# Performance work log

Hardware: AMD Instinct MI355X
Metric: run time of the kernel (lower is better)

The kernel has to match this reference:

```python
import jax, jax.numpy as jnp
import numpy as np

EPS = 1e-5

def _bn(x, gamma, beta):
    # BatchNorm1d training-mode math: batch mean / biased variance over edge dim
    mean = jnp.mean(x, axis=0)
    var = jnp.mean(jnp.square(x - mean), axis=0)
    return (x - mean) * (gamma / jnp.sqrt(var + EPS)) + beta


def setup_inputs() -> dict:
    key = jax.random.key(0)
    ks = jax.random.split(key, 12)
    n, d, s, h, e = 50000, 256, 32, 128, 500000
    feat = 3 * d + s + 1  # 801
    sc = lambda fan_in: 1.0 / np.sqrt(fan_in)
    return {
        "node_embeddings": jax.random.normal(ks[0], (n, d), jnp.float32),
        "gradient_scores": jax.random.normal(ks[1], (e,), jnp.float32),
        "step_embedding": jax.random.normal(ks[2], (s,), jnp.float32),
        "W1": jax.random.normal(ks[3], (feat, h), jnp.float32) * sc(feat),
        "b1": jnp.zeros((h,), jnp.float32),
        "g1": jnp.ones((h,), jnp.float32),
        "be1": jnp.zeros((h,), jnp.float32),
        "W2": jax.random.normal(ks[4], (h, h // 2), jnp.float32) * sc(h),
        "b2": jnp.zeros((h // 2,), jnp.float32),
        "g2": jnp.ones((h // 2,), jnp.float32),
        "be2": jnp.zeros((h // 2,), jnp.float32),
        "W3": jax.random.normal(ks[5], (h // 2, 1), jnp.float32) * sc(h // 2),
        "b3": jnp.zeros((1,), jnp.float32),
        "edge_index": jax.random.randint(ks[6], (2, e), 0, n, jnp.int64),
    }


def reference(node_embeddings, gradient_scores, step_embedding,
              W1, b1, g1, be1, W2, b2, g2, be2, W3, b3, edge_index):
    src, dst = edge_index[0], edge_index[1]
    h_u = node_embeddings[src]              # [E, d]
    h_v = node_embeddings[dst]              # [E, d]
    edge_diff = jnp.abs(h_u - h_v)          # [E, d]
    E = edge_index.shape[1]
    step = jnp.broadcast_to(step_embedding[None, :], (E, step_embedding.shape[0]))
    feats = jnp.concatenate([h_u, h_v, edge_diff, step, gradient_scores[:, None]], axis=1)
    x = jnp.maximum(feats @ W1 + b1, 0.0)
    x = _bn(x, g1, be1)                     # dropout is identity in eval
    x = jnp.maximum(x @ W2 + b2, 0.0)
    x = _bn(x, g2, be2)
    out = jnp.tanh(x @ W3 + b3)[:, 0]       # [E]
    return out
```

## Files before the change

kernel.cpp:

```cpp
#include <hip/hip_runtime.h>

#define NE 500000
#define DIMK 256
#define H1 128
#define H2 64
#define EPSBN 1e-5f
#define GRID1 512
#define NT1 1954
#define NJOBS2 NT1

typedef _Float16 half8 __attribute__((ext_vector_type(8)));
typedef float f32x4 __attribute__((ext_vector_type(4)));
typedef unsigned short ushort8 __attribute__((ext_vector_type(8)));

static __device__ __forceinline__ half8 habs8(half8 x) {
  ushort8 u = __builtin_bit_cast(ushort8, x);
  u &= (unsigned short)0x7FFF;
  return __builtin_bit_cast(half8, u);
}
static __device__ __forceinline__ float h2f(unsigned int u) {
  return (float)__builtin_bit_cast(_Float16, (unsigned short)(u & 0xffff));
}

__global__ void k_prep(const float* __restrict__ W1, const float* __restrict__ b1,
                       const float* __restrict__ step, float* __restrict__ c0) {
  const int j = threadIdx.x;
  if (j < H1) {
    float a = b1[j];
#pragma unroll
    for (int tt = 0; tt < 32; ++tt) a += step[tt] * W1[(768 + tt) * H1 + j];
    c0[j] = a;
  }
}

__global__ void k_prep16(const float* __restrict__ emb, _Float16* __restrict__ embh) {
  const int i = (blockIdx.x * 256 + threadIdx.x) * 8;
  const float4 a = *(const float4*)(emb + i);
  const float4 b = *(const float4*)(emb + i + 4);
  half8 h;
  h[0] = (_Float16)a.x; h[1] = (_Float16)a.y; h[2] = (_Float16)a.z; h[3] = (_Float16)a.w;
  h[4] = (_Float16)b.x; h[5] = (_Float16)b.y; h[6] = (_Float16)b.z; h[7] = (_Float16)b.w;
  *(half8*)(embh + i) = h;
}

__global__ void k_prepB(const float* __restrict__ W1, _Float16* __restrict__ bfrag) {
  const int g = blockIdx.x * 256 + threadIdx.x;
  const int lane = g & 63, f = g >> 6;
  const int c = f & 7, kc = (f >> 3) & 7, s = f >> 6;
  const int row0 = s * 256 + kc * 32 + (lane >> 4) * 8;
  const int col = c * 16 + (lane & 15);
  half8 h;
#pragma unroll
  for (int j = 0; j < 8; ++j) h[j] = (_Float16)W1[(row0 + j) * H1 + col];
  *(half8*)(bfrag + (size_t)g * 8) = h;
}

__global__ __launch_bounds__(256, 2)
void k_layer1(const _Float16* __restrict__ embh, const void* __restrict__ eidx_raw,
              const float* __restrict__ grad, const float* __restrict__ W1,
              const float* __restrict__ c0, const _Float16* __restrict__ bfrag,
              _Float16* __restrict__ x1, float* __restrict__ p1) {
  __shared__ int s_src[256], s_dst[256];
  __shared__ float s_g[256];
  __shared__ float s_wg[128], s_c0[128], s_sum[128], s_sq[128];

  const int t = threadIdx.x, bid = blockIdx.x;
  const int w = t >> 6, lane = t & 63, quad = lane >> 4, m15 = lane & 15;

  if (t < 128) {
    s_wg[t] = W1[800 * H1 + t];
    s_c0[t] = c0[t];
    s_sum[t] = 0.f; s_sq[t] = 0.f;
  }

  const unsigned* ew = (const unsigned*)eidx_raw;
  const bool is64 = ((ew[1] | ew[3] | ew[5] | ew[7]) == 0u);
  const int* e32 = (const int*)eidx_raw;
  const long long* e64 = (const long long*)eidx_raw;

  float st_s[8] = {0, 0, 0, 0, 0, 0, 0, 0}, st_q[8] = {0, 0, 0, 0, 0, 0, 0, 0};
  const half8* bp = (const half8*)bfrag;

  for (int tile = bid; tile < NT1; tile += GRID1) {
    const int base = tile * 256;
    __syncthreads();
    {
      int e = base + t; if (e >= NE) e = NE - 1;
      if (is64) { s_src[t] = (int)e64[e]; s_dst[t] = (int)e64[NE + e]; }
      else      { s_src[t] = e32[e];      s_dst[t] = e32[NE + e]; }
      s_g[t] = grad[e];
    }
    __syncthreads();

    const int r0 = w * 64 + m15;
    const _Float16* pu[4];
    const _Float16* pv[4];
#pragma unroll
    for (int r = 0; r < 4; ++r) {
      pu[r] = embh + (size_t)s_src[r0 + r * 16] * DIMK + quad * 8;
      pv[r] = embh + (size_t)s_dst[r0 + r * 16] * DIMK + quad * 8;
    }
    f32x4 acc[4][8];
#pragma unroll
    for (int r = 0; r < 4; ++r)
#pragma unroll
      for (int c = 0; c < 8; ++c) acc[r][c] = (f32x4)0.f;

#pragma unroll 1
    for (int kc = 0; kc < 8; ++kc) {
      half8 u[4], v[4], d[4];
#pragma unroll
      for (int r = 0; r < 4; ++r) {
        u[r] = *(const half8*)(pu[r] + kc * 32);
        v[r] = *(const half8*)(pv[r] + kc * 32);
      }
#pragma unroll
      for (int r = 0; r < 4; ++r) d[r] = habs8(u[r] - v[r]);

      half8 bu = bp[(kc * 8 + 0) * 64 + lane];
      half8 bv = bp[(64 + kc * 8 + 0) * 64 + lane];
      half8 bd = bp[(128 + kc * 8 + 0) * 64 + lane];
#pragma unroll
      for (int c = 0; c < 8; ++c) {
        half8 nbu, nbv, nbd;
        if (c < 7) {
          nbu = bp[(kc * 8 + c + 1) * 64 + lane];
          nbv = bp[(64 + kc * 8 + c + 1) * 64 + lane];
          nbd = bp[(128 + kc * 8 + c + 1) * 64 + lane];
        }
#pragma unroll
        for (int r = 0; r < 4; ++r)
          acc[r][c] = __builtin_amdgcn_mfma_f32_16x16x32_f16(u[r], bu, acc[r][c], 0, 0, 0);
#pragma unroll
        for (int r = 0; r < 4; ++r)
          acc[r][c] = __builtin_amdgcn_mfma_f32_16x16x32_f16(v[r], bv, acc[r][c], 0, 0, 0);
#pragma unroll
        for (int r = 0; r < 4; ++r)
          acc[r][c] = __builtin_amdgcn_mfma_f32_16x16x32_f16(d[r], bd, acc[r][c], 0, 0, 0);
        if (c < 7) { bu = nbu; bv = nbv; bd = nbd; }
      }
    }
#pragma unroll
    for (int r = 0; r < 4; ++r) {
      const int erow = w * 64 + r * 16 + quad * 4;
#pragma unroll
      for (int c = 0; c < 8; ++c) {
        const int colL = c * 16 + m15;
        const float wgv = s_wg[colL], c0v = s_c0[colL];
#pragma unroll
        for (int reg = 0; reg < 4; ++reg) {
          const int e = base + erow + reg;
          float x = acc[r][c][reg] + s_g[erow + reg] * wgv + c0v;
          x = fmaxf(x, 0.f);
          if (e >= NE) x = 0.f;
          st_s[c] += x; st_q[c] += x * x;
          if (e < NE) x1[(size_t)e * H1 + colL] = (_Float16)x;
        }
      }
    }
  }
  __syncthreads();
#pragma unroll
  for (int c = 0; c < 8; ++c) {
    float a = st_s[c]; a += __shfl_xor(a, 16); a += __shfl_xor(a, 32);
    float b = st_q[c]; b += __shfl_xor(b, 16); b += __shfl_xor(b, 32);
    if (lane < 16) { atomicAdd(&s_sum[c * 16 + m15], a); atomicAdd(&s_sq[c * 16 + m15], b); }
  }
  __syncthreads();
  if (t < 128) {
    p1[t * GRID1 + bid] = s_sum[t];
    p1[128 * GRID1 + t * GRID1 + bid] = s_sq[t];
  }
}

__global__ void k_fin1(const float* __restrict__ p1, const float* __restrict__ g1,
                       const float* __restrict__ be1, const float* __restrict__ W2,
                       const float* __restrict__ b2, float* __restrict__ w2f,
                       float* __restrict__ b2f) {
  __shared__ float s1[128], t1[128];
  const int t = threadIdx.x;
  if (t < 128) {
    float s = 0.f, q = 0.f;
    const float4* rs = (const float4*)(p1 + t * GRID1);
    const float4* rq = (const float4*)(p1 + 128 * GRID1 + t * GRID1);
#pragma unroll 4
    for (int i = 0; i < GRID1 / 4; ++i) {
      float4 a = rs[i]; s += a.x + a.y + a.z + a.w;
      float4 b = rq[i]; q += b.x + b.y + b.z + b.w;
    }
    const float inv = 1.0f / (float)NE;
    float mean = s * inv;
    float var = q * inv - mean * mean;
    float sc = g1[t] * rsqrtf(var + EPSBN);
    s1[t] = sc; t1[t] = be1[t] - mean * sc;
  }
  __syncthreads();
  for (int i = t; i < H1 * H2; i += 256) w2f[i] = s1[i >> 6] * W2[i];
  if (t < 64) {
    float b = b2[t];
    for (int j = 0; j < 128; ++j) b += t1[j] * W2[j * 64 + t];
    b2f[t] = b;
  }
}

__global__ __launch_bounds__(256, 2)
void k_layer2(const _Float16* __restrict__ x1, const float* __restrict__ w2f,
              const float* __restrict__ b2f, _Float16* __restrict__ x2,
              float* __restrict__ p2) {
  __shared__ __align__(16) _Float16 b_lds[8192];
  __shared__ float s_b[64], s_sum[64], s_sq[64];
  const int t = threadIdx.x, bid = blockIdx.x;
  const int w = t >> 6, lane = t & 63, quad = lane >> 4, m15 = lane & 15;

  for (int i = t; i < 8192; i += 256) {
    const int j = i & 7, li = (i >> 3) & 63, f = i >> 9;
    const int c = f & 3, kk = f >> 2;
    const int row = kk * 32 + (li >> 4) * 8 + j;
    const int col = c * 16 + (li & 15);
    b_lds[i] = (_Float16)w2f[row * H2 + col];
  }
  if (t < 64) { s_b[t] = b2f[t]; s_sum[t] = 0.f; s_sq[t] = 0.f; }
  __syncthreads();

  float st_s[4] = {0, 0, 0, 0}, st_q[4] = {0, 0, 0, 0};
  const half8* bp = (const half8*)b_lds;

  for (int job = bid; job < NJOBS2; job += GRID1) {
    const int base = job * 256;
    const _Float16* pa[4];
#pragma unroll
    for (int r = 0; r < 4; ++r) {
      int e = base + w * 64 + r * 16 + m15; if (e >= NE) e = NE - 1;
      pa[r] = x1 + (size_t)e * H1 + quad * 8;
    }
    f32x4 acc[4][4];
#pragma unroll
    for (int r = 0; r < 4; ++r)
#pragma unroll
      for (int c = 0; c < 4; ++c) acc[r][c] = (f32x4)0.f;

#pragma unroll
    for (int kk = 0; kk < 4; ++kk) {
      half8 a[4];
#pragma unroll
      for (int r = 0; r < 4; ++r) a[r] = *(const half8*)(pa[r] + kk * 32);
#pragma unroll
      for (int c = 0; c < 4; ++c) {
        const half8 bf = bp[(kk * 4 + c) * 64 + lane];
#pragma unroll
        for (int r = 0; r < 4; ++r)
          acc[r][c] = __builtin_amdgcn_mfma_f32_16x16x32_f16(a[r], bf, acc[r][c], 0, 0, 0);
      }
    }
#pragma unroll
    for (int r = 0; r < 4; ++r) {
      const int erow = w * 64 + r * 16 + quad * 4;
#pragma unroll
      for (int c = 0; c < 4; ++c) {
        const int colL = c * 16 + m15;
        const float bv = s_b[colL];
#pragma unroll
        for (int reg = 0; reg < 4; ++reg) {
          const int e = base + erow + reg;
          float x = acc[r][c][reg] + bv;
          x = fmaxf(x, 0.f);
          if (e >= NE) x = 0.f;
          st_s[c] += x; st_q[c] += x * x;
          if (e < NE) x2[(size_t)e * H2 + colL] = (_Float16)x;
        }
      }
    }
  }
  __syncthreads();
#pragma unroll
  for (int c = 0; c < 4; ++c) {
    float a = st_s[c]; a += __shfl_xor(a, 16); a += __shfl_xor(a, 32);
    float b = st_q[c]; b += __shfl_xor(b, 16); b += __shfl_xor(b, 32);
    if (lane < 16) { atomicAdd(&s_sum[c * 16 + m15], a); atomicAdd(&s_sq[c * 16 + m15], b); }
  }
  __syncthreads();
  if (t < 64) {
    p2[t * 512 + bid] = s_sum[t];
    p2[64 * 512 + t * 512 + bid] = s_sq[t];
  }
}

__global__ void k_fin2(const float* __restrict__ p2, const float* __restrict__ g2,
                       const float* __restrict__ be2, const float* __restrict__ W3,
                       const float* __restrict__ b3, float* __restrict__ w3f,
                       float* __restrict__ b3f) {
  __shared__ float tp[64];
  const int t = threadIdx.x;
  if (t < 64) {
    float s = 0.f, q = 0.f;
    const float4* rs = (const float4*)(p2 + t * 512);
    const float4* rq = (const float4*)(p2 + 64 * 512 + t * 512);
#pragma unroll 4
    for (int i = 0; i < 128; ++i) {
      float4 a = rs[i]; s += a.x + a.y + a.z + a.w;
      float4 b = rq[i]; q += b.x + b.y + b.z + b.w;
    }
    const float inv = 1.0f / (float)NE;
    float mean = s * inv;
    float var = q * inv - mean * mean;
    float sc = g2[t] * rsqrtf(var + EPSBN);
    float tt = be2[t] - mean * sc;
    w3f[t] = sc * W3[t];
    tp[t] = tt * W3[t];
  }
  __syncthreads();
  if (t == 0) {
    float b = b3[0];
    for (int j = 0; j < 64; ++j) b += tp[j];
    b3f[0] = b;
  }
}

__global__ __launch_bounds__(256)
void k_out(const unsigned short* __restrict__ x2, const float* __restrict__ w3f,
           const float* __restrict__ b3f, float* __restrict__ out) {
  __shared__ float s_w[64];
  __shared__ float s_b;
  const int t = threadIdx.x;
  if (t < 64) s_w[t] = w3f[t];
  if (t == 0) s_b = b3f[0];
  __syncthreads();
  const int gid = blockIdx.x * 256 + t;
  const int e = gid >> 2, p = gid & 3;
  if (e < NE) {
    const uint4* r = (const uint4*)(x2 + (size_t)e * H2 + p * 16);
    float s = 0.f;
#pragma unroll
    for (int i = 0; i < 2; ++i) {
      const uint4 u = r[i];
      const int jb = p * 16 + i * 8;
      s += h2f(u.x) * s_w[jb + 0] + h2f(u.x >> 16) * s_w[jb + 1];
      s += h2f(u.y) * s_w[jb + 2] + h2f(u.y >> 16) * s_w[jb + 3];
      s += h2f(u.z) * s_w[jb + 4] + h2f(u.z >> 16) * s_w[jb + 5];
      s += h2f(u.w) * s_w[jb + 6] + h2f(u.w >> 16) * s_w[jb + 7];
    }
    s += __shfl_xor(s, 1);
    s += __shfl_xor(s, 2);
    if (p == 0) out[e] = tanhf(s + s_b);
  }
}

extern "C" void kernel_launch(void* const* d_in, const int* in_sizes, int n_in,
                              void* d_out, int out_size, void* d_ws, size_t ws_size,
                              hipStream_t stream) {
  const float* emb  = (const float*)d_in[0];
  const float* grad = (const float*)d_in[1];
  const float* step = (const float*)d_in[2];
  const float* W1   = (const float*)d_in[3];
  const float* b1   = (const float*)d_in[4];
  const float* g1   = (const float*)d_in[5];
  const float* be1  = (const float*)d_in[6];
  const float* W2   = (const float*)d_in[7];
  const float* b2   = (const float*)d_in[8];
  const float* g2   = (const float*)d_in[9];
  const float* be2  = (const float*)d_in[10];
  const float* W3   = (const float*)d_in[11];
  const float* b3   = (const float*)d_in[12];
  const void*  eidx = (const void*)d_in[13];
  float* out = (float*)d_out;

  char* ws = (char*)d_ws;
  _Float16* embh  = (_Float16*)(ws + 0);
  _Float16* x2    = (_Float16*)(ws + 0);
  _Float16* bfrag = (_Float16*)(ws + 25600000LL);
  float*    c0    = (float*)(ws + 25796608LL);
  _Float16* x1    = (_Float16*)(ws + 64000000LL);
  float* p1  = (float*)(ws + 192000000LL);
  float* p2  = (float*)(ws + 192524288LL);
  float* w2f = (float*)(ws + 192786432LL);
  float* b2f = (float*)(ws + 192819200LL);
  float* w3f = (float*)(ws + 192819456LL);
  float* b3f = (float*)(ws + 192819712LL);

  k_prep  <<<1,    256, 0, stream>>>(W1, b1, step, c0);
  k_prep16<<<6250, 256, 0, stream>>>(emb, embh);
  k_prepB <<<48,   256, 0, stream>>>(W1, bfrag);
  k_layer1<<<GRID1,256, 0, stream>>>(embh, eidx, grad, W1, c0, bfrag, x1, p1);
  k_fin1  <<<1,    256, 0, stream>>>(p1, g1, be1, W2, b2, w2f, b2f);
  k_layer2<<<GRID1,256, 0, stream>>>(x1, w2f, b2f, x2, p2);
  k_fin2  <<<1,    128, 0, stream>>>(p2, g2, be2, W3, b3, w3f, b3f);
  k_out   <<<7813, 256, 0, stream>>>((const unsigned short*)x2, w3f, b3f, out);
}
```

Before: 383.8 us.

## Stage W1 fragments in LDS and split layer1 output columns across block pairs

Layer1 now runs 256 blocks of 1024 threads. Each pair of blocks owns a 64-column half of the hidden layer, and each block stages its half of the W1 B-fragments (96 KB) in LDS instead of streaming them from global memory. Every block covers 512-edge tiles, with each wave computing 32 rows by 64 columns, so the edge gathers are duplicated across the two column halves. Layer2 gets a grid of 1024, and the partial-statistic buffers are resized to match. The cost is redundant embedding gathers and large LDS use, which limits occupancy; the gain is less global and L2 traffic for the weights and lower register pressure.

```diff
diff --git a/kernel.cpp b/kernel.cpp
--- a/kernel.cpp
+++ b/kernel.cpp
@@ -5,9 +5,9 @@
 #define H1 128
 #define H2 64
 #define EPSBN 1e-5f
-#define GRID1 512
-#define NT1 1954
-#define NJOBS2 NT1
+#define NT1 977
+#define GRID2 1024
+#define NJOBS2 1954
 
 typedef _Float16 half8 __attribute__((ext_vector_type(8)));
 typedef float f32x4 __attribute__((ext_vector_type(4)));
@@ -55,21 +55,32 @@
   *(half8*)(bfrag + (size_t)g * 8) = h;
 }
 
-__global__ __launch_bounds__(256, 2)
+__global__ __launch_bounds__(1024, 4)
 void k_layer1(const _Float16* __restrict__ embh, const void* __restrict__ eidx_raw,
               const float* __restrict__ grad, const float* __restrict__ W1,
               const float* __restrict__ c0, const _Float16* __restrict__ bfrag,
               _Float16* __restrict__ x1, float* __restrict__ p1) {
-  __shared__ int s_src[256], s_dst[256];
-  __shared__ float s_g[256];
-  __shared__ float s_wg[128], s_c0[128], s_sum[128], s_sq[128];
+  __shared__ __align__(16) _Float16 ldsB[49152];
+  __shared__ int s_src[512], s_dst[512];
+  __shared__ float s_g[512];
+  __shared__ float s_wg[64], s_c0[64], s_sum[64], s_sq[64];
 
   const int t = threadIdx.x, bid = blockIdx.x;
+  const int ch = bid & 1;
   const int w = t >> 6, lane = t & 63, quad = lane >> 4, m15 = lane & 15;
 
-  if (t < 128) {
-    s_wg[t] = W1[800 * H1 + t];
-    s_c0[t] = c0[t];
+  {
+    const half8* gb = (const half8*)bfrag;
+    half8* lb = (half8*)ldsB;
+    for (int i = t; i < 6144; i += 1024) {
+      const int li = i & 63, fl = i >> 6;
+      const int c = fl & 3, kc = (fl >> 2) & 7, s = fl >> 5;
+      lb[i] = gb[(size_t)((s * 64 + kc * 8 + ch * 4 + c) * 64 + li)];
+    }
+  }
+  if (t < 64) {
+    s_wg[t] = W1[800 * H1 + ch * 64 + t];
+    s_c0[t] = c0[ch * 64 + t];
     s_sum[t] = 0.f; s_sq[t] = 0.f;
   }
 
@@ -78,13 +89,13 @@
   const int* e32 = (const int*)eidx_raw;
   const long long* e64 = (const long long*)eidx_raw;
 
-  float st_s[8] = {0, 0, 0, 0, 0, 0, 0, 0}, st_q[8] = {0, 0, 0, 0, 0, 0, 0, 0};
-  const half8* bp = (const half8*)bfrag;
-
-  for (int tile = bid; tile < NT1; tile += GRID1) {
-    const int base = tile * 256;
+  float st_s[4] = {0, 0, 0, 0}, st_q[4] = {0, 0, 0, 0};
+  const half8* lb = (const half8*)ldsB;
+
+  for (int tile = (bid >> 1); tile < NT1; tile += 128) {
+    const int base = tile * 512;
     __syncthreads();
-    {
+    if (t < 512) {
       int e = base + t; if (e >= NE) e = NE - 1;
       if (is64) { s_src[t] = (int)e64[e]; s_dst[t] = (int)e64[NE + e]; }
       else      { s_src[t] = e32[e];      s_dst[t] = e32[NE + e]; }
@@ -92,84 +103,70 @@
     }
     __syncthreads();
 
-    const int r0 = w * 64 + m15;
-    const _Float16* pu[4];
-    const _Float16* pv[4];
-#pragma unroll
-    for (int r = 0; r < 4; ++r) {
-      pu[r] = embh + (size_t)s_src[r0 + r * 16] * DIMK + quad * 8;
-      pv[r] = embh + (size_t)s_dst[r0 + r * 16] * DIMK + quad * 8;
-    }
-    f32x4 acc[4][8];
-#pragma unroll
-    for (int r = 0; r < 4; ++r)
-#pragma unroll
-      for (int c = 0; c < 8; ++c) acc[r][c] = (f32x4)0.f;
+    const int row0 = w * 32 + m15;
+    const _Float16* pu0 = embh + (size_t)s_src[row0] * DIMK + quad * 8;
+    const _Float16* pv0 = embh + (size_t)s_dst[row0] * DIMK + quad * 8;
+    const _Float16* pu1 = embh + (size_t)s_src[row0 + 16] * DIMK + quad * 8;
+    const _Float16* pv1 = embh + (size_t)s_dst[row0 + 16] * DIMK + quad * 8;
+
+    f32x4 acc[2][4];
+#pragma unroll
+    for (int r = 0; r < 2; ++r)
+#pragma unroll
+      for (int c = 0; c < 4; ++c) acc[r][c] = (f32x4)0.f;
 
 #pragma unroll 1
     for (int kc = 0; kc < 8; ++kc) {
-      half8 u[4], v[4], d[4];
-#pragma unroll
-      for (int r = 0; r < 4; ++r) {
-        u[r] = *(const half8*)(pu[r] + kc * 32);
-        v[r] = *(const half8*)(pv[r] + kc * 32);
+      const half8 u0 = *(const half8*)(pu0 + kc * 32);
+      const half8 v0 = *(const half8*)(pv0 + kc * 32);
+      const half8 u1 = *(const half8*)(pu1 + kc * 32);
+      const half8 v1 = *(const half8*)(pv1 + kc * 32);
+      const half8 d0 = habs8(u0 - v0);
+      const half8 d1 = habs8(u1 - v1);
+#pragma unroll
+      for (int c = 0; c < 4; ++c) {
+        const half8 bu = lb[((0 * 8 + kc) * 4 + c) * 64 + lane];
+        const half8 bv = lb[((1 * 8 + kc) * 4 + c) * 64 + lane];
+        const half8 bd = lb[((2 * 8 + kc) * 4 + c) * 64 + lane];
+        acc[0][c] = __builtin_amdgcn_mfma_f32_16x16x32_f16(u0, bu, acc[0][c], 0, 0, 0);
+        acc[1][c] = __builtin_amdgcn_mfma_f32_16x16x32_f16(u1, bu, acc[1][c], 0, 0, 0);
+        acc[0][c] = __builtin_amdgcn_mfma_f32_16x16x32_f16(v0, bv, acc[0][c], 0, 0, 0);
+        acc[1][c] = __builtin_amdgcn_mfma_f32_16x16x32_f16(v1, bv, acc[1][c], 0, 0, 0);
+        acc[0][c] = __builtin_amdgcn_mfma_f32_16x16x32_f16(d0, bd, acc[0][c], 0, 0, 0);
+        acc[1][c] = __builtin_amdgcn_mfma_f32_16x16x32_f16(d1, bd, acc[1][c], 0, 0, 0);
       }
-#pragma unroll
-      for (int r = 0; r < 4; ++r) d[r] = habs8(u[r] - v[r]);
-
-      half8 bu = bp[(kc * 8 + 0) * 64 + lane];
-      half8 bv = bp[(64 + kc * 8 + 0) * 64 + lane];
-      half8 bd = bp[(128 + kc * 8 + 0) * 64 + lane];
-#pragma unroll
-      for (int c = 0; c < 8; ++c) {
-        half8 nbu, nbv, nbd;
-        if (c < 7) {
-          nbu = bp[(kc * 8 + c + 1) * 64 + lane];
-          nbv = bp[(64 + kc * 8 + c + 1) * 64 + lane];
-          nbd = bp[(128 + kc * 8 + c + 1) * 64 + lane];
-        }
-#pragma unroll
-        for (int r = 0; r < 4; ++r)
-          acc[r][c] = __builtin_amdgcn_mfma_f32_16x16x32_f16(u[r], bu, acc[r][c], 0, 0, 0);
-#pragma unroll
-        for (int r = 0; r < 4; ++r)
-          acc[r][c] = __builtin_amdgcn_mfma_f32_16x16x32_f16(v[r], bv, acc[r][c], 0, 0, 0);
-#pragma unroll
-        for (int r = 0; r < 4; ++r)
-          acc[r][c] = __builtin_amdgcn_mfma_f32_16x16x32_f16(d[r], bd, acc[r][c], 0, 0, 0);
-        if (c < 7) { bu = nbu; bv = nbv; bd = nbd; }
-      }
-    }
-#pragma unroll
-    for (int r = 0; r < 4; ++r) {
-      const int erow = w * 64 + r * 16 + quad * 4;
-#pragma unroll
-      for (int c = 0; c < 8; ++c) {
+    }
+#pragma unroll
+    for (int r = 0; r < 2; ++r) {
+      const int rrow = w * 32 + r * 16 + quad * 4;
+#pragma unroll
+      for (int c = 0; c < 4; ++c) {
         const int colL = c * 16 + m15;
         const float wgv = s_wg[colL], c0v = s_c0[colL];
 #pragma unroll
         for (int reg = 0; reg < 4; ++reg) {
-          const int e = base + erow + reg;
-          float x = acc[r][c][reg] + s_g[erow + reg] * wgv + c0v;
+          const int e = base + rrow + reg;
+          float x = acc[r][c][reg] + s_g[rrow + reg] * wgv + c0v;
           x = fmaxf(x, 0.f);
           if (e >= NE) x = 0.f;
           st_s[c] += x; st_q[c] += x * x;
-          if (e < NE) x1[(size_t)e * H1 + colL] = (_Float16)x;
+          if (e < NE) x1[(size_t)e * H1 + ch * 64 + colL] = (_Float16)x;
         }
       }
     }
   }
   __syncthreads();
 #pragma unroll
-  for (int c = 0; c < 8; ++c) {
+  for (int c = 0; c < 4; ++c) {
     float a = st_s[c]; a += __shfl_xor(a, 16); a += __shfl_xor(a, 32);
     float b = st_q[c]; b += __shfl_xor(b, 16); b += __shfl_xor(b, 32);
     if (lane < 16) { atomicAdd(&s_sum[c * 16 + m15], a); atomicAdd(&s_sq[c * 16 + m15], b); }
   }
   __syncthreads();
-  if (t < 128) {
-    p1[t * GRID1 + bid] = s_sum[t];
-    p1[128 * GRID1 + t * GRID1 + bid] = s_sq[t];
+  if (t < 64) {
+    const int colG = ch * 64 + t, bh = bid >> 1;
+    p1[colG * 128 + bh] = s_sum[t];
+    p1[128 * 128 + colG * 128 + bh] = s_sq[t];
   }
 }
 
@@ -181,10 +178,10 @@
   const int t = threadIdx.x;
   if (t < 128) {
     float s = 0.f, q = 0.f;
-    const float4* rs = (const float4*)(p1 + t * GRID1);
-    const float4* rq = (const float4*)(p1 + 128 * GRID1 + t * GRID1);
+    const float4* rs = (const float4*)(p1 + t * 128);
+    const float4* rq = (const float4*)(p1 + 128 * 128 + t * 128);
 #pragma unroll 4
-    for (int i = 0; i < GRID1 / 4; ++i) {
+    for (int i = 0; i < 32; ++i) {
       float4 a = rs[i]; s += a.x + a.y + a.z + a.w;
       float4 b = rq[i]; q += b.x + b.y + b.z + b.w;
     }
@@ -225,7 +222,7 @@
   float st_s[4] = {0, 0, 0, 0}, st_q[4] = {0, 0, 0, 0};
   const half8* bp = (const half8*)b_lds;
 
-  for (int job = bid; job < NJOBS2; job += GRID1) {
+  for (int job = bid; job < NJOBS2; job += GRID2) {
     const int base = job * 256;
     const _Float16* pa[4];
 #pragma unroll
@@ -280,8 +277,8 @@
   }
   __syncthreads();
   if (t < 64) {
-    p2[t * 512 + bid] = s_sum[t];
-    p2[64 * 512 + t * 512 + bid] = s_sq[t];
+    p2[t * GRID2 + bid] = s_sum[t];
+    p2[64 * GRID2 + t * GRID2 + bid] = s_sq[t];
   }
 }
 
@@ -293,10 +290,10 @@
   const int t = threadIdx.x;
   if (t < 64) {
     float s = 0.f, q = 0.f;
-    const float4* rs = (const float4*)(p2 + t * 512);
-    const float4* rq = (const float4*)(p2 + 64 * 512 + t * 512);
+    const float4* rs = (const float4*)(p2 + t * GRID2);
+    const float4* rq = (const float4*)(p2 + 64 * GRID2 + t * GRID2);
 #pragma unroll 4
-    for (int i = 0; i < 128; ++i) {
+    for (int i = 0; i < GRID2 / 4; ++i) {
       float4 a = rs[i]; s += a.x + a.y + a.z + a.w;
       float4 b = rq[i]; q += b.x + b.y + b.z + b.w;
     }
@@ -371,18 +368,18 @@
   float*    c0    = (float*)(ws + 25796608LL);
   _Float16* x1    = (_Float16*)(ws + 64000000LL);
   float* p1  = (float*)(ws + 192000000LL);
-  float* p2  = (float*)(ws + 192524288LL);
-  float* w2f = (float*)(ws + 192786432LL);
-  float* b2f = (float*)(ws + 192819200LL);
-  float* w3f = (float*)(ws + 192819456LL);
-  float* b3f = (float*)(ws + 192819712LL);
+  float* p2  = (float*)(ws + 192131072LL);
+  float* w2f = (float*)(ws + 192655360LL);
+  float* b2f = (float*)(ws + 192688128LL);
+  float* w3f = (float*)(ws + 192688384LL);
+  float* b3f = (float*)(ws + 192688640LL);
 
   k_prep  <<<1,    256, 0, stream>>>(W1, b1, step, c0);
   k_prep16<<<6250, 256, 0, stream>>>(emb, embh);
   k_prepB <<<48,   256, 0, stream>>>(W1, bfrag);
-  k_layer1<<<GRID1,256, 0, stream>>>(embh, eidx, grad, W1, c0, bfrag, x1, p1);
+  k_layer1<<<256, 1024, 0, stream>>>(embh, eidx, grad, W1, c0, bfrag, x1, p1);
   k_fin1  <<<1,    256, 0, stream>>>(p1, g1, be1, W2, b2, w2f, b2f);
-  k_layer2<<<GRID1,256, 0, stream>>>(x1, w2f, b2f, x2, p2);
+  k_layer2<<<GRID2,256, 0, stream>>>(x1, w2f, b2f, x2, p2);
   k_fin2  <<<1,    128, 0, stream>>>(p2, g2, be2, W3, b3, w3f, b3f);
   k_out   <<<7813, 256, 0, stream>>>((const unsigned short*)x2, w3f, b3f, out);
 }
```

Measured after the change: 405.5 us. 1.06x slower.

## Counting-sort edges by source node to improve gather locality

Applied to the files above, without the earlier changes.

Adds a histogram, a single-block scan and an atomic scatter that reorder edges by source node, so layer1 gathers the source embeddings from contiguous rows and gets better cache reuse. The original edge id is kept and used to scatter outputs back to their original positions. Layer2 now writes its result in place into the x1 buffer with the H1 stride, which removes the separate x2 buffer. The cost is four extra kernels, one of them a serial scan over 50k nodes in a single block, plus a scattered final write.

```diff
diff --git a/kernel.cpp b/kernel.cpp
--- a/kernel.cpp
+++ b/kernel.cpp
@@ -1,13 +1,14 @@
 #include <hip/hip_runtime.h>
 
 #define NE 500000
+#define ND 50000
 #define DIMK 256
 #define H1 128
 #define H2 64
 #define EPSBN 1e-5f
 #define GRID1 512
 #define NT1 1954
-#define NJOBS2 NT1
+#define GRID2 512
 
 typedef _Float16 half8 __attribute__((ext_vector_type(8)));
 typedef float f32x4 __attribute__((ext_vector_type(4)));
@@ -20,6 +21,59 @@
 }
 static __device__ __forceinline__ float h2f(unsigned int u) {
   return (float)__builtin_bit_cast(_Float16, (unsigned short)(u & 0xffff));
+}
+
+__global__ void k_zero(int* __restrict__ hist) {
+  const int i = blockIdx.x * 1024 + threadIdx.x;
+  if (i < ND) hist[i] = 0;
+}
+
+__global__ void k_hist(const void* __restrict__ eidx, int* __restrict__ hist) {
+  const int e = blockIdx.x * 1024 + threadIdx.x;
+  if (e >= NE) return;
+  const unsigned* ew = (const unsigned*)eidx;
+  const bool is64 = ((ew[1] | ew[3] | ew[5] | ew[7]) == 0u);
+  const int s = is64 ? (int)((const long long*)eidx)[e] : ((const int*)eidx)[e];
+  atomicAdd(&hist[s], 1);
+}
+
+__global__ void k_scan(const int* __restrict__ hist, int* __restrict__ offs,
+                       int* __restrict__ cursor) {
+  __shared__ int sc[1024];
+  const int t = threadIdx.x;
+  int run = 0;
+  for (int c0 = 0; c0 < ND; c0 += 1024) {
+    const int i = c0 + t;
+    const int v = (i < ND) ? hist[i] : 0;
+    sc[t] = v;
+    __syncthreads();
+    for (int off = 1; off < 1024; off <<= 1) {
+      int x = (t >= off) ? sc[t - off] : 0;
+      __syncthreads();
+      sc[t] += x;
+      __syncthreads();
+    }
+    const int incl = sc[t];
+    const int total = sc[1023];
+    if (i < ND) { offs[i] = run + incl - v; cursor[i] = run + incl - v; }
+    run += total;
+    __syncthreads();
+  }
+}
+
+__global__ void k_scatter(const void* __restrict__ eidx, const float* __restrict__ grad,
+                          int* __restrict__ cursor, int* __restrict__ srcs,
+                          int* __restrict__ dsts, float* __restrict__ grads,
+                          int* __restrict__ oeid) {
+  const int e = blockIdx.x * 1024 + threadIdx.x;
+  if (e >= NE) return;
+  const unsigned* ew = (const unsigned*)eidx;
+  const bool is64 = ((ew[1] | ew[3] | ew[5] | ew[7]) == 0u);
+  int s, d;
+  if (is64) { s = (int)((const long long*)eidx)[e]; d = (int)((const long long*)eidx)[NE + e]; }
+  else      { s = ((const int*)eidx)[e];            d = ((const int*)eidx)[NE + e]; }
+  const int p = atomicAdd(&cursor[s], 1);
+  srcs[p] = s; dsts[p] = d; grads[p] = grad[e]; oeid[p] = e;
 }
 
 __global__ void k_prep(const float* __restrict__ W1, const float* __restrict__ b1,
@@ -56,10 +110,11 @@
 }
 
 __global__ __launch_bounds__(256, 2)
-void k_layer1(const _Float16* __restrict__ embh, const void* __restrict__ eidx_raw,
-              const float* __restrict__ grad, const float* __restrict__ W1,
-              const float* __restrict__ c0, const _Float16* __restrict__ bfrag,
-              _Float16* __restrict__ x1, float* __restrict__ p1) {
+void k_layer1(const _Float16* __restrict__ embh, const int* __restrict__ srcs,
+              const int* __restrict__ dsts, const float* __restrict__ grads,
+              const float* __restrict__ W1, const float* __restrict__ c0,
+              const _Float16* __restrict__ bfrag, _Float16* __restrict__ x1,
+              float* __restrict__ p1) {
   __shared__ int s_src[256], s_dst[256];
   __shared__ float s_g[256];
   __shared__ float s_wg[128], s_c0[128], s_sum[128], s_sq[128];
@@ -72,11 +127,6 @@
     s_c0[t] = c0[t];
     s_sum[t] = 0.f; s_sq[t] = 0.f;
   }
-
-  const unsigned* ew = (const unsigned*)eidx_raw;
-  const bool is64 = ((ew[1] | ew[3] | ew[5] | ew[7]) == 0u);
-  const int* e32 = (const int*)eidx_raw;
-  const long long* e64 = (const long long*)eidx_raw;
 
   float st_s[8] = {0, 0, 0, 0, 0, 0, 0, 0}, st_q[8] = {0, 0, 0, 0, 0, 0, 0, 0};
   const half8* bp = (const half8*)bfrag;
@@ -86,9 +136,9 @@
     __syncthreads();
     {
       int e = base + t; if (e >= NE) e = NE - 1;
-      if (is64) { s_src[t] = (int)e64[e]; s_dst[t] = (int)e64[NE + e]; }
-      else      { s_src[t] = e32[e];      s_dst[t] = e32[NE + e]; }
-      s_g[t] = grad[e];
+      s_src[t] = srcs[e];
+      s_dst[t] = dsts[e];
+      s_g[t] = grads[e];
     }
     __syncthreads();
 
@@ -204,9 +254,8 @@
 }
 
 __global__ __launch_bounds__(256, 2)
-void k_layer2(const _Float16* __restrict__ x1, const float* __restrict__ w2f,
-              const float* __restrict__ b2f, _Float16* __restrict__ x2,
-              float* __restrict__ p2) {
+void k_layer2(_Float16* __restrict__ x1, const float* __restrict__ w2f,
+              const float* __restrict__ b2f, float* __restrict__ p2) {
   __shared__ __align__(16) _Float16 b_lds[8192];
   __shared__ float s_b[64], s_sum[64], s_sq[64];
   const int t = threadIdx.x, bid = blockIdx.x;
@@ -225,7 +274,7 @@
   float st_s[4] = {0, 0, 0, 0}, st_q[4] = {0, 0, 0, 0};
   const half8* bp = (const half8*)b_lds;
 
-  for (int job = bid; job < NJOBS2; job += GRID1) {
+  for (int job = bid; job < NT1; job += GRID2) {
     const int base = job * 256;
     const _Float16* pa[4];
 #pragma unroll
@@ -266,7 +315,7 @@
           x = fmaxf(x, 0.f);
           if (e >= NE) x = 0.f;
           st_s[c] += x; st_q[c] += x * x;
-          if (e < NE) x2[(size_t)e * H2 + colL] = (_Float16)x;
+          if (e < NE) x1[(size_t)e * H1 + colL] = (_Float16)x;
         }
       }
     }
@@ -280,8 +329,8 @@
   }
   __syncthreads();
   if (t < 64) {
-    p2[t * 512 + bid] = s_sum[t];
-    p2[64 * 512 + t * 512 + bid] = s_sq[t];
+    p2[t * GRID2 + bid] = s_sum[t];
+    p2[64 * GRID2 + t * GRID2 + bid] = s_sq[t];
   }
 }
 
@@ -293,10 +342,10 @@
   const int t = threadIdx.x;
   if (t < 64) {
     float s = 0.f, q = 0.f;
-    const float4* rs = (const float4*)(p2 + t * 512);
-    const float4* rq = (const float4*)(p2 + 64 * 512 + t * 512);
+    const float4* rs = (const float4*)(p2 + t * GRID2);
+    const float4* rq = (const float4*)(p2 + 64 * GRID2 + t * GRID2);
 #pragma unroll 4
-    for (int i = 0; i < 128; ++i) {
+    for (int i = 0; i < GRID2 / 4; ++i) {
       float4 a = rs[i]; s += a.x + a.y + a.z + a.w;
       float4 b = rq[i]; q += b.x + b.y + b.z + b.w;
     }
@@ -317,8 +366,9 @@
 }
 
 __global__ __launch_bounds__(256)
-void k_out(const unsigned short* __restrict__ x2, const float* __restrict__ w3f,
-           const float* __restrict__ b3f, float* __restrict__ out) {
+void k_out(const unsigned short* __restrict__ x2, const int* __restrict__ oeid,
+           const float* __restrict__ w3f, const float* __restrict__ b3f,
+           float* __restrict__ out) {
   __shared__ float s_w[64];
   __shared__ float s_b;
   const int t = threadIdx.x;
@@ -328,7 +378,7 @@
   const int gid = blockIdx.x * 256 + t;
   const int e = gid >> 2, p = gid & 3;
   if (e < NE) {
-    const uint4* r = (const uint4*)(x2 + (size_t)e * H2 + p * 16);
+    const uint4* r = (const uint4*)(x2 + (size_t)e * H1 + p * 16);
     float s = 0.f;
 #pragma unroll
     for (int i = 0; i < 2; ++i) {
@@ -341,7 +391,7 @@
     }
     s += __shfl_xor(s, 1);
     s += __shfl_xor(s, 2);
-    if (p == 0) out[e] = tanhf(s + s_b);
+    if (p == 0) out[oeid[e]] = tanhf(s + s_b);
   }
 }
 
@@ -366,10 +416,16 @@
 
   char* ws = (char*)d_ws;
   _Float16* embh  = (_Float16*)(ws + 0);
-  _Float16* x2    = (_Float16*)(ws + 0);
   _Float16* bfrag = (_Float16*)(ws + 25600000LL);
   float*    c0    = (float*)(ws + 25796608LL);
-  _Float16* x1    = (_Float16*)(ws + 64000000LL);
+  int*   hist   = (int*)(ws + 25800000LL);
+  int*   offs   = (int*)(ws + 26000000LL);
+  int*   cursor = (int*)(ws + 26200000LL);
+  int*   srcs   = (int*)(ws + 26400000LL);
+  int*   dsts   = (int*)(ws + 28400000LL);
+  float* grads  = (float*)(ws + 30400000LL);
+  int*   oeid   = (int*)(ws + 32400000LL);
+  _Float16* x1  = (_Float16*)(ws + 64000000LL);
   float* p1  = (float*)(ws + 192000000LL);
   float* p2  = (float*)(ws + 192524288LL);
   float* w2f = (float*)(ws + 192786432LL);
@@ -377,12 +433,16 @@
   float* w3f = (float*)(ws + 192819456LL);
   float* b3f = (float*)(ws + 192819712LL);
 
-  k_prep  <<<1,    256, 0, stream>>>(W1, b1, step, c0);
-  k_prep16<<<6250, 256, 0, stream>>>(emb, embh);
-  k_prepB <<<48,   256, 0, stream>>>(W1, bfrag);
-  k_layer1<<<GRID1,256, 0, stream>>>(embh, eidx, grad, W1, c0, bfrag, x1, p1);
-  k_fin1  <<<1,    256, 0, stream>>>(p1, g1, be1, W2, b2, w2f, b2f);
-  k_layer2<<<GRID1,256, 0, stream>>>(x1, w2f, b2f, x2, p2);
-  k_fin2  <<<1,    128, 0, stream>>>(p2, g2, be2, W3, b3, w3f, b3f);
-  k_out   <<<7813, 256, 0, stream>>>((const unsigned short*)x2, w3f, b3f, out);
-}
+  k_zero   <<<49,  1024, 0, stream>>>(hist);
+  k_hist   <<<489, 1024, 0, stream>>>(eidx, hist);
+  k_scan   <<<1,   1024, 0, stream>>>(hist, offs, cursor);
+  k_scatter<<<489, 1024, 0, stream>>>(eidx, grad, cursor, srcs, dsts, grads, oeid);
+  k_prep   <<<1,    256, 0, stream>>>(W1, b1, step, c0);
+  k_prep16 <<<6250, 256, 0, stream>>>(emb, embh);
+  k_prepB  <<<48,   256, 0, stream>>>(W1, bfrag);
+  k_layer1 <<<GRID1,256, 0, stream>>>(embh, srcs, dsts, grads, W1, c0, bfrag, x1, p1);
+  k_fin1   <<<1,    256, 0, stream>>>(p1, g1, be1, W2, b2, w2f, b2f);
+  k_layer2 <<<GRID2,256, 0, stream>>>(x1, w2f, b2f, p2);
+  k_fin2   <<<1,    128, 0, stream>>>(p2, g2, be2, W3, b3, w3f, b3f);
+  k_out    <<<7813, 256, 0, stream>>>((const unsigned short*)x1, oeid, w3f, b3f, out);
+}
```

Measured after the change: 526.4 us. +37.2%, slower.

## Precompute per-node W1 projections and only run per-edge GEMM on abs-diff

Applied to the files above, without the earlier changes.

Splits layer-1's matmul: the h_u and h_v parts of feats@W1 are computed once per node (50k rows) into a PQ table, and the edge kernel only multiplies the |h_u-h_v| slice with W1 held in LDS. A separate stats pass and layer 2 rebuild the pre-activation by gathering P[src]+Q[dst]+E, so the gathers run again but the per-edge GEMM work drops by two thirds. The extra reads and the fp16 summation of the three terms may cost some precision, and E is reused as the buffer for x2.

```diff
diff --git a/kernel.cpp b/kernel.cpp
--- a/kernel.cpp
+++ b/kernel.cpp
@@ -1,13 +1,16 @@
 #include <hip/hip_runtime.h>
 
 #define NE 500000
+#define ND 50000
 #define DIMK 256
 #define H1 128
 #define H2 64
 #define EPSBN 1e-5f
-#define GRID1 512
-#define NT1 1954
-#define NJOBS2 NT1
+#define NT 1954
+#define NTN 196
+#define GE 512
+#define GS 512
+#define G2 1024
 
 typedef _Float16 half8 __attribute__((ext_vector_type(8)));
 typedef float f32x4 __attribute__((ext_vector_type(4)));
@@ -17,6 +20,12 @@
   ushort8 u = __builtin_bit_cast(ushort8, x);
   u &= (unsigned short)0x7FFF;
   return __builtin_bit_cast(half8, u);
+}
+static __device__ __forceinline__ half8 hrelu8(half8 x) {
+  half8 r;
+#pragma unroll
+  for (int j = 0; j < 8; ++j) r[j] = x[j] > (_Float16)0 ? x[j] : (_Float16)0;
+  return r;
 }
 static __device__ __forceinline__ float h2f(unsigned int u) {
   return (float)__builtin_bit_cast(_Float16, (unsigned short)(u & 0xffff));
@@ -43,48 +52,118 @@
   *(half8*)(embh + i) = h;
 }
 
-__global__ void k_prepB(const float* __restrict__ W1, _Float16* __restrict__ bfrag) {
+__global__ void k_prepBC(const float* __restrict__ W1, _Float16* __restrict__ bfragC) {
   const int g = blockIdx.x * 256 + threadIdx.x;
   const int lane = g & 63, f = g >> 6;
-  const int c = f & 7, kc = (f >> 3) & 7, s = f >> 6;
-  const int row0 = s * 256 + kc * 32 + (lane >> 4) * 8;
+  const int c = f & 7, kc = f >> 3;
+  const int row0 = 512 + kc * 32 + (lane >> 4) * 8;
   const int col = c * 16 + (lane & 15);
   half8 h;
 #pragma unroll
   for (int j = 0; j < 8; ++j) h[j] = (_Float16)W1[(row0 + j) * H1 + col];
-  *(half8*)(bfrag + (size_t)g * 8) = h;
+  *(half8*)(bfragC + (size_t)g * 8) = h;
+}
+
+__global__ void k_prepBN(const float* __restrict__ W1, _Float16* __restrict__ bfragN) {
+  const int g = blockIdx.x * 256 + threadIdx.x;
+  const int lane = g & 63, f = g >> 6;
+  const int c = f & 15, kc = f >> 4;
+  const int k0 = kc * 32 + (lane >> 4) * 8;
+  const int colg = c * 16 + (lane & 15);
+  half8 h;
+#pragma unroll
+  for (int j = 0; j < 8; ++j) {
+    const int k = k0 + j;
+    h[j] = (_Float16)((colg < 128) ? W1[k * H1 + colg] : W1[(256 + k) * H1 + (colg - 128)]);
+  }
+  *(half8*)(bfragN + (size_t)g * 8) = h;
 }
 
 __global__ __launch_bounds__(256, 2)
-void k_layer1(const _Float16* __restrict__ embh, const void* __restrict__ eidx_raw,
-              const float* __restrict__ grad, const float* __restrict__ W1,
-              const float* __restrict__ c0, const _Float16* __restrict__ bfrag,
-              _Float16* __restrict__ x1, float* __restrict__ p1) {
+void k_node(const _Float16* __restrict__ embh, const _Float16* __restrict__ bfragN,
+            _Float16* __restrict__ PQ) {
+  __shared__ __align__(16) _Float16 lB[16384];
+  const int t = threadIdx.x, bid = blockIdx.x;
+  const int ch = bid & 3, tile = bid >> 2;
+  const int w = t >> 6, lane = t & 63, quad = lane >> 4, m15 = lane & 15;
+  {
+    half8* lb = (half8*)lB; const half8* gb = (const half8*)bfragN;
+    for (int i = t; i < 2048; i += 256) {
+      const int li = i & 63, fl = i >> 6;
+      const int c = fl & 3, kc = fl >> 2;
+      lb[i] = gb[(size_t)((kc * 16 + ch * 4 + c) * 64 + li)];
+    }
+  }
+  __syncthreads();
+  const int base = tile * 256;
+  const _Float16* pa[4];
+#pragma unroll
+  for (int r = 0; r < 4; ++r) {
+    int n = base + w * 64 + r * 16 + m15; if (n >= ND) n = ND - 1;
+    pa[r] = embh + (size_t)n * DIMK + quad * 8;
+  }
+  f32x4 acc[4][4];
+#pragma unroll
+  for (int r = 0; r < 4; ++r)
+#pragma unroll
+    for (int c = 0; c < 4; ++c) acc[r][c] = (f32x4)0.f;
+  const half8* lb = (const half8*)lB;
+#pragma unroll 1
+  for (int kc = 0; kc < 8; ++kc) {
+    half8 a[4];
+#pragma unroll
+    for (int r = 0; r < 4; ++r) a[r] = *(const half8*)(pa[r] + kc * 32);
+#pragma unroll
+    for (int c = 0; c < 4; ++c) {
+      const half8 bf = lb[(kc * 4 + c) * 64 + lane];
+#pragma unroll
+      for (int r = 0; r < 4; ++r)
+        acc[r][c] = __builtin_amdgcn_mfma_f32_16x16x32_f16(a[r], bf, acc[r][c], 0, 0, 0);
+    }
+  }
+#pragma unroll
+  for (int r = 0; r < 4; ++r) {
+    const int nrow = base + w * 64 + r * 16 + quad * 4;
+#pragma unroll
+    for (int c = 0; c < 4; ++c) {
+      const int col = ch * 64 + c * 16 + m15;
+#pragma unroll
+      for (int reg = 0; reg < 4; ++reg) {
+        const int n = nrow + reg;
+        if (n < ND) PQ[(size_t)n * 256 + col] = (_Float16)acc[r][c][reg];
+      }
+    }
+  }
+}
+
+__global__ __launch_bounds__(512, 4)
+void k_edge(const _Float16* __restrict__ embh, const void* __restrict__ eidx_raw,
+            const float* __restrict__ grad, const float* __restrict__ W1,
+            const float* __restrict__ c0, const _Float16* __restrict__ bfragC,
+            _Float16* __restrict__ E) {
+  __shared__ __align__(16) _Float16 lB[32768];
   __shared__ int s_src[256], s_dst[256];
   __shared__ float s_g[256];
-  __shared__ float s_wg[128], s_c0[128], s_sum[128], s_sq[128];
-
+  __shared__ float s_wg[128], s_c0[128];
   const int t = threadIdx.x, bid = blockIdx.x;
   const int w = t >> 6, lane = t & 63, quad = lane >> 4, m15 = lane & 15;
-
-  if (t < 128) {
-    s_wg[t] = W1[800 * H1 + t];
-    s_c0[t] = c0[t];
-    s_sum[t] = 0.f; s_sq[t] = 0.f;
-  }
+  const int rw = w & 3, cw = w >> 2;
+  {
+    half8* lb = (half8*)lB; const half8* gb = (const half8*)bfragC;
+    for (int i = t; i < 4096; i += 512) lb[i] = gb[i];
+  }
+  if (t < 128) { s_wg[t] = W1[800 * H1 + t]; s_c0[t] = c0[t]; }
 
   const unsigned* ew = (const unsigned*)eidx_raw;
   const bool is64 = ((ew[1] | ew[3] | ew[5] | ew[7]) == 0u);
   const int* e32 = (const int*)eidx_raw;
   const long long* e64 = (const long long*)eidx_raw;
-
-  float st_s[8] = {0, 0, 0, 0, 0, 0, 0, 0}, st_q[8] = {0, 0, 0, 0, 0, 0, 0, 0};
-  const half8* bp = (const half8*)bfrag;
-
-  for (int tile = bid; tile < NT1; tile += GRID1) {
+  const half8* lb = (const half8*)lB;
+
+  for (int tile = bid; tile < NT; tile += GE) {
     const int base = tile * 256;
     __syncthreads();
-    {
+    if (t < 256) {
       int e = base + t; if (e >= NE) e = NE - 1;
       if (is64) { s_src[t] = (int)e64[e]; s_dst[t] = (int)e64[NE + e]; }
       else      { s_src[t] = e32[e];      s_dst[t] = e32[NE + e]; }
@@ -92,84 +171,91 @@
     }
     __syncthreads();
 
-    const int r0 = w * 64 + m15;
     const _Float16* pu[4];
     const _Float16* pv[4];
 #pragma unroll
     for (int r = 0; r < 4; ++r) {
-      pu[r] = embh + (size_t)s_src[r0 + r * 16] * DIMK + quad * 8;
-      pv[r] = embh + (size_t)s_dst[r0 + r * 16] * DIMK + quad * 8;
-    }
-    f32x4 acc[4][8];
+      const int row = rw * 64 + r * 16 + m15;
+      pu[r] = embh + (size_t)s_src[row] * DIMK + quad * 8;
+      pv[r] = embh + (size_t)s_dst[row] * DIMK + quad * 8;
+    }
+    f32x4 acc[4][4];
 #pragma unroll
     for (int r = 0; r < 4; ++r)
 #pragma unroll
-      for (int c = 0; c < 8; ++c) acc[r][c] = (f32x4)0.f;
+      for (int c = 0; c < 4; ++c) acc[r][c] = (f32x4)0.f;
 
 #pragma unroll 1
     for (int kc = 0; kc < 8; ++kc) {
-      half8 u[4], v[4], d[4];
+      half8 d[4];
 #pragma unroll
       for (int r = 0; r < 4; ++r) {
-        u[r] = *(const half8*)(pu[r] + kc * 32);
-        v[r] = *(const half8*)(pv[r] + kc * 32);
-      }
-#pragma unroll
-      for (int r = 0; r < 4; ++r) d[r] = habs8(u[r] - v[r]);
-
-      half8 bu = bp[(kc * 8 + 0) * 64 + lane];
-      half8 bv = bp[(64 + kc * 8 + 0) * 64 + lane];
-      half8 bd = bp[(128 + kc * 8 + 0) * 64 + lane];
-#pragma unroll
-      for (int c = 0; c < 8; ++c) {
-        half8 nbu, nbv, nbd;
-        if (c < 7) {
-          nbu = bp[(kc * 8 + c + 1) * 64 + lane];
-          nbv = bp[(64 + kc * 8 + c + 1) * 64 + lane];
-          nbd = bp[(128 + kc * 8 + c + 1) * 64 + lane];
-        }
-#pragma unroll
-        for (int r = 0; r < 4; ++r)
-          acc[r][c] = __builtin_amdgcn_mfma_f32_16x16x32_f16(u[r], bu, acc[r][c], 0, 0, 0);
-#pragma unroll
-        for (int r = 0; r < 4; ++r)
-          acc[r][c] = __builtin_amdgcn_mfma_f32_16x16x32_f16(v[r], bv, acc[r][c], 0, 0, 0);
+        const half8 u = *(const half8*)(pu[r] + kc * 32);
+        const half8 v = *(const half8*)(pv[r] + kc * 32);
+        d[r] = habs8(u - v);
+      }
+#pragma unroll
+      for (int c = 0; c < 4; ++c) {
+        const half8 bd = lb[(kc * 8 + cw * 4 + c) * 64 + lane];
 #pragma unroll
         for (int r = 0; r < 4; ++r)
           acc[r][c] = __builtin_amdgcn_mfma_f32_16x16x32_f16(d[r], bd, acc[r][c], 0, 0, 0);
-        if (c < 7) { bu = nbu; bv = nbv; bd = nbd; }
       }
     }
 #pragma unroll
     for (int r = 0; r < 4; ++r) {
-      const int erow = w * 64 + r * 16 + quad * 4;
-#pragma unroll
-      for (int c = 0; c < 8; ++c) {
-        const int colL = c * 16 + m15;
+      const int erow = rw * 64 + r * 16 + quad * 4;
+#pragma unroll
+      for (int c = 0; c < 4; ++c) {
+        const int colL = cw * 64 + c * 16 + m15;
         const float wgv = s_wg[colL], c0v = s_c0[colL];
 #pragma unroll
         for (int reg = 0; reg < 4; ++reg) {
           const int e = base + erow + reg;
-          float x = acc[r][c][reg] + s_g[erow + reg] * wgv + c0v;
-          x = fmaxf(x, 0.f);
-          if (e >= NE) x = 0.f;
-          st_s[c] += x; st_q[c] += x * x;
-          if (e < NE) x1[(size_t)e * H1 + colL] = (_Float16)x;
+          const float x = acc[r][c][reg] + s_g[erow + reg] * wgv + c0v;
+          if (e < NE) E[(size_t)e * H1 + colL] = (_Float16)x;
         }
       }
     }
   }
-  __syncthreads();
-#pragma unroll
-  for (int c = 0; c < 8; ++c) {
-    float a = st_s[c]; a += __shfl_xor(a, 16); a += __shfl_xor(a, 32);
-    float b = st_q[c]; b += __shfl_xor(b, 16); b += __shfl_xor(b, 32);
-    if (lane < 16) { atomicAdd(&s_sum[c * 16 + m15], a); atomicAdd(&s_sq[c * 16 + m15], b); }
+}
+
+__global__ __launch_bounds__(256, 4)
+void k_stats(const _Float16* __restrict__ E, const _Float16* __restrict__ PQ,
+             const void* __restrict__ eidx_raw, float* __restrict__ p1) {
+  __shared__ float s_sum[128], s_sq[128];
+  const int t = threadIdx.x, bid = blockIdx.x;
+  const int cg = t & 15, el = t >> 4;
+  if (t < 128) { s_sum[t] = 0.f; s_sq[t] = 0.f; }
+  __syncthreads();
+  const unsigned* ew = (const unsigned*)eidx_raw;
+  const bool is64 = ((ew[1] | ew[3] | ew[5] | ew[7]) == 0u);
+  const int* e32 = (const int*)eidx_raw;
+  const long long* e64 = (const long long*)eidx_raw;
+  float s8[8] = {0, 0, 0, 0, 0, 0, 0, 0}, q8[8] = {0, 0, 0, 0, 0, 0, 0, 0};
+  for (int e = bid * 16 + el; e < NE; e += GS * 16) {
+    int sr, dr;
+    if (is64) { sr = (int)e64[e]; dr = (int)e64[NE + e]; }
+    else      { sr = e32[e];      dr = e32[NE + e]; }
+    const half8 E8 = *(const half8*)(E + (size_t)e * H1 + cg * 8);
+    const half8 P8 = *(const half8*)(PQ + (size_t)sr * 256 + cg * 8);
+    const half8 Q8 = *(const half8*)(PQ + (size_t)dr * 256 + 128 + cg * 8);
+    const half8 x = E8 + P8 + Q8;
+#pragma unroll
+    for (int j = 0; j < 8; ++j) {
+      const float xf = fmaxf((float)x[j], 0.f);
+      s8[j] += xf; q8[j] += xf * xf;
+    }
+  }
+#pragma unroll
+  for (int j = 0; j < 8; ++j) {
+    atomicAdd(&s_sum[cg * 8 + j], s8[j]);
+    atomicAdd(&s_sq[cg * 8 + j], q8[j]);
   }
   __syncthreads();
   if (t < 128) {
-    p1[t * GRID1 + bid] = s_sum[t];
-    p1[128 * GRID1 + t * GRID1 + bid] = s_sq[t];
+    p1[t * GS + bid] = s_sum[t];
+    p1[128 * GS + t * GS + bid] = s_sq[t];
   }
 }
 
@@ -181,10 +267,10 @@
   const int t = threadIdx.x;
   if (t < 128) {
     float s = 0.f, q = 0.f;
-    const float4* rs = (const float4*)(p1 + t * GRID1);
-    const float4* rq = (const float4*)(p1 + 128 * GRID1 + t * GRID1);
+    const float4* rs = (const float4*)(p1 + t * GS);
+    const float4* rq = (const float4*)(p1 + 128 * GS + t * GS);
 #pragma unroll 4
-    for (int i = 0; i < GRID1 / 4; ++i) {
+    for (int i = 0; i < GS / 4; ++i) {
       float4 a = rs[i]; s += a.x + a.y + a.z + a.w;
       float4 b = rq[i]; q += b.x + b.y + b.z + b.w;
     }
@@ -203,11 +289,12 @@
   }
 }
 
-__global__ __launch_bounds__(256, 2)
-void k_layer2(const _Float16* __restrict__ x1, const float* __restrict__ w2f,
-              const float* __restrict__ b2f, _Float16* __restrict__ x2,
-              float* __restrict__ p2) {
+__global__ __launch_bounds__(256, 4)
+void k_layer2(_Float16* __restrict__ E, const _Float16* __restrict__ PQ,
+              const void* __restrict__ eidx_raw, const float* __restrict__ w2f,
+              const float* __restrict__ b2f, float* __restrict__ p2) {
   __shared__ __align__(16) _Float16 b_lds[8192];
+  __shared__ int s_src[256], s_dst[256];
   __shared__ float s_b[64], s_sum[64], s_sq[64];
   const int t = threadIdx.x, bid = blockIdx.x;
   const int w = t >> 6, lane = t & 63, quad = lane >> 4, m15 = lane & 15;
@@ -220,18 +307,35 @@
     b_lds[i] = (_Float16)w2f[row * H2 + col];
   }
   if (t < 64) { s_b[t] = b2f[t]; s_sum[t] = 0.f; s_sq[t] = 0.f; }
-  __syncthreads();
+
+  const unsigned* ew = (const unsigned*)eidx_raw;
+  const bool is64 = ((ew[1] | ew[3] | ew[5] | ew[7]) == 0u);
+  const int* e32 = (const int*)eidx_raw;
+  const long long* e64 = (const long long*)eidx_raw;
 
   float st_s[4] = {0, 0, 0, 0}, st_q[4] = {0, 0, 0, 0};
   const half8* bp = (const half8*)b_lds;
 
-  for (int job = bid; job < NJOBS2; job += GRID1) {
+  for (int job = bid; job < NT; job += G2) {
     const int base = job * 256;
-    const _Float16* pa[4];
+    __syncthreads();
+    if (t < 256) {
+      int e = base + t; if (e >= NE) e = NE - 1;
+      if (is64) { s_src[t] = (int)e64[e]; s_dst[t] = (int)e64[NE + e]; }
+      else      { s_src[t] = e32[e];      s_dst[t] = e32[NE + e]; }
+    }
+    __syncthreads();
+
+    const _Float16* pe[4];
+    const _Float16* ps[4];
+    const _Float16* pq[4];
 #pragma unroll
     for (int r = 0; r < 4; ++r) {
-      int e = base + w * 64 + r * 16 + m15; if (e >= NE) e = NE - 1;
-      pa[r] = x1 + (size_t)e * H1 + quad * 8;
+      const int row = w * 64 + r * 16 + m15;
+      int e = base + row; if (e >= NE) e = NE - 1;
+      pe[r] = E + (size_t)e * H1 + quad * 8;
+      ps[r] = PQ + (size_t)s_src[row] * 256 + quad * 8;
+      pq[r] = PQ + (size_t)s_dst[row] * 256 + 128 + quad * 8;
     }
     f32x4 acc[4][4];
 #pragma unroll
@@ -243,7 +347,12 @@
     for (int kk = 0; kk < 4; ++kk) {
       half8 a[4];
 #pragma unroll
-      for (int r = 0; r < 4; ++r) a[r] = *(const half8*)(pa[r] + kk * 32);
+      for (int r = 0; r < 4; ++r) {
+        const half8 e8 = *(const half8*)(pe[r] + kk * 32);
+        const half8 p8 = *(const half8*)(ps[r] + kk * 32);
+        const half8 q8 = *(const half8*)(pq[r] + kk * 32);
+        a[r] = hrelu8(e8 + p8 + q8);
+      }
 #pragma unroll
       for (int c = 0; c < 4; ++c) {
         const half8 bf = bp[(kk * 4 + c) * 64 + lane];
@@ -266,7 +375,7 @@
           x = fmaxf(x, 0.f);
           if (e >= NE) x = 0.f;
           st_s[c] += x; st_q[c] += x * x;
-          if (e < NE) x2[(size_t)e * H2 + colL] = (_Float16)x;
+          if (e < NE) E[(size_t)e * H1 + colL] = (_Float16)x;
         }
       }
     }
@@ -280,8 +389,8 @@
   }
   __syncthreads();
   if (t < 64) {
-    p2[t * 512 + bid] = s_sum[t];
-    p2[64 * 512 + t * 512 + bid] = s_sq[t];
+    p2[t * G2 + bid] = s_sum[t];
+    p2[64 * G2 + t * G2 + bid] = s_sq[t];
   }
 }
 
@@ -293,10 +402,10 @@
   const int t = threadIdx.x;
   if (t < 64) {
     float s = 0.f, q = 0.f;
-    const float4* rs = (const float4*)(p2 + t * 512);
-    const float4* rq = (const float4*)(p2 + 64 * 512 + t * 512);
+    const float4* rs = (const float4*)(p2 + t * G2);
+    const float4* rq = (const float4*)(p2 + 64 * G2 + t * G2);
 #pragma unroll 4
-    for (int i = 0; i < 128; ++i) {
+    for (int i = 0; i < G2 / 4; ++i) {
       float4 a = rs[i]; s += a.x + a.y + a.z + a.w;
       float4 b = rq[i]; q += b.x + b.y + b.z + b.w;
     }
@@ -328,7 +437,7 @@
   const int gid = blockIdx.x * 256 + t;
   const int e = gid >> 2, p = gid & 3;
   if (e < NE) {
-    const uint4* r = (const uint4*)(x2 + (size_t)e * H2 + p * 16);
+    const uint4* r = (const uint4*)(x2 + (size_t)e * H1 + p * 16);
     float s = 0.f;
 #pragma unroll
     for (int i = 0; i < 2; ++i) {
@@ -365,24 +474,28 @@
   float* out = (float*)d_out;
 
   char* ws = (char*)d_ws;
-  _Float16* embh  = (_Float16*)(ws + 0);
-  _Float16* x2    = (_Float16*)(ws + 0);
-  _Float16* bfrag = (_Float16*)(ws + 25600000LL);
-  float*    c0    = (float*)(ws + 25796608LL);
-  _Float16* x1    = (_Float16*)(ws + 64000000LL);
-  float* p1  = (float*)(ws + 192000000LL);
-  float* p2  = (float*)(ws + 192524288LL);
-  float* w2f = (float*)(ws + 192786432LL);
-  float* b2f = (float*)(ws + 192819200LL);
-  float* w3f = (float*)(ws + 192819456LL);
-  float* b3f = (float*)(ws + 192819712LL);
-
-  k_prep  <<<1,    256, 0, stream>>>(W1, b1, step, c0);
-  k_prep16<<<6250, 256, 0, stream>>>(emb, embh);
-  k_prepB <<<48,   256, 0, stream>>>(W1, bfrag);
-  k_layer1<<<GRID1,256, 0, stream>>>(embh, eidx, grad, W1, c0, bfrag, x1, p1);
-  k_fin1  <<<1,    256, 0, stream>>>(p1, g1, be1, W2, b2, w2f, b2f);
-  k_layer2<<<GRID1,256, 0, stream>>>(x1, w2f, b2f, x2, p2);
-  k_fin2  <<<1,    128, 0, stream>>>(p2, g2, be2, W3, b3, w3f, b3f);
-  k_out   <<<7813, 256, 0, stream>>>((const unsigned short*)x2, w3f, b3f, out);
-}
+  _Float16* embh   = (_Float16*)(ws + 0);
+  _Float16* PQ     = (_Float16*)(ws + 25600000LL);
+  _Float16* bfragC = (_Float16*)(ws + 51200000LL);
+  _Float16* bfragN = (_Float16*)(ws + 51265536LL);
+  float*    c0     = (float*)(ws + 51396608LL);
+  float*    w2f    = (float*)(ws + 51397120LL);
+  float*    b2f    = (float*)(ws + 51429888LL);
+  float*    w3f    = (float*)(ws + 51430144LL);
+  float*    b3f    = (float*)(ws + 51430400LL);
+  float*    p1     = (float*)(ws + 51500032LL);
+  float*    p2     = (float*)(ws + 52024320LL);
+  _Float16* E      = (_Float16*)(ws + 64000000LL);
+
+  k_prep   <<<1,    256, 0, stream>>>(W1, b1, step, c0);
+  k_prep16 <<<6250, 256, 0, stream>>>(emb, embh);
+  k_prepBC <<<16,   256, 0, stream>>>(W1, bfragC);
+  k_prepBN <<<32,   256, 0, stream>>>(W1, bfragN);
+  k_node   <<<NTN * 4, 256, 0, stream>>>(embh, bfragN, PQ);
+  k_edge   <<<GE,   512, 0, stream>>>(embh, eidx, grad, W1, c0, bfragC, E);
+  k_stats  <<<GS,   256, 0, stream>>>(E, PQ, eidx, p1);
+  k_fin1   <<<1,    256, 0, stream>>>(p1, g1, be1, W2, b2, w2f, b2f);
+  k_layer2 <<<G2,   256, 0, stream>>>(E, PQ, eidx, w2f, b2f, p2);
+  k_fin2   <<<1,    128, 0, stream>>>(p2, g2, be2, W3, b3, w3f, b3f);
+  k_out    <<<7813, 256, 0, stream>>>((const unsigned short*)E, w3f, b3f, out);
+}
```

After: 562.7 us. 46.6% more time.
